# Optimization experiments

Hardware: AMD Instinct MI355X
Metric: run time of the kernel (lower is better)

Reference implementation:

```python
import jax, jax.numpy as jnp
import numpy as np

B, T, C, H = 8, 2048, 1024, 64


def build_rope_cache(seq_len, dim):
    half = dim // 2
    inv_freq = 1.0 / (10000.0 ** (jnp.arange(half, dtype=jnp.float32) / half))
    t = jnp.arange(seq_len, dtype=jnp.float32)
    freqs = t[:, None] * inv_freq[None, :]          # (T, half)
    cos = jnp.repeat(jnp.cos(freqs), 2, axis=-1)    # (T, dim) interleaved
    sin = jnp.repeat(jnp.sin(freqs), 2, axis=-1)
    return cos, sin


def apply_rope(x, cos, sin):
    # x: (B, T, H); cos/sin: (T, H)
    x1 = x[..., ::2]
    x2 = x[..., 1::2]
    rot = jnp.stack([-x2, x1], axis=-1).reshape(x.shape)
    return x * cos[None] + rot * sin[None]


def setup_inputs() -> dict:
    key = jax.random.key(0)
    kx, kq, kk, kv = jax.random.split(key, 4)
    scale = 1.0 / np.sqrt(C)
    return {
        "x": jax.random.normal(kx, (B, T, C), dtype=jnp.float32),
        "Wq": jax.random.normal(kq, (C, H), dtype=jnp.float32) * scale,
        "Wk": jax.random.normal(kk, (C, H), dtype=jnp.float32) * scale,
        "Wv": jax.random.normal(kv, (C, H), dtype=jnp.float32) * scale,
    }


def reference(x, Wq, Wk, Wv):
    Bc, Tc, _ = x.shape
    head_size = Wq.shape[1]
    cos, sin = build_rope_cache(Tc, head_size)

    q = apply_rope(x @ Wq, cos, sin)   # (B, T, H)
    k = apply_rope(x @ Wk, cos, sin)   # (B, T, H)
    v = x @ Wv                          # (B, T, H)

    # full TxT masked softmax attention (matches original non-fused path)
    wei = jnp.einsum('bth,bsh->bts', q, k) * (head_size ** -0.5)  # (B, T, T)
    causal = jnp.tril(jnp.ones((Tc, Tc), dtype=bool))
    wei = jnp.where(causal[None], wei, -jnp.inf)
    wei = jax.nn.softmax(wei, axis=-1)
    # dropout p=0 (eval mode) -> identity
    return jnp.einsum('bts,bsh->bth', wei, v)
```

## Files before the change

kernel.cpp:

```cpp
#include <hip/hip_runtime.h>
#include <cmath>

#define Tn  2048
#define Cn  1024
#define Hn  64
#define BTn 16384

typedef _Float16 f16x8 __attribute__((ext_vector_type(8)));
typedef _Float16 f16x4 __attribute__((ext_vector_type(4)));
typedef _Float16 f16x2 __attribute__((ext_vector_type(2)));
typedef float    f32x4 __attribute__((ext_vector_type(4)));

#define MFMA16(a, b, c) __builtin_amdgcn_mfma_f32_16x16x32_f16(a, b, c, 0, 0, 0)

__global__ __launch_bounds__(256) void prep_w_kernel(
    const float* __restrict__ Wq, const float* __restrict__ Wk,
    const float* __restrict__ Wv, _Float16* __restrict__ Wt)
{
    __shared__ float ts[64][65];
    const int blk = blockIdx.x;
    const int p   = blk >> 4;
    const int c0  = (blk & 15) * 64;
    const float* __restrict__ W = (p == 0) ? Wq : (p == 1) ? Wk : Wv;
    const int tid = threadIdx.x;
    #pragma unroll
    for (int it = 0; it < 16; it++) {
        int idx = tid + it * 256;
        int c = idx >> 6, n = idx & 63;
        ts[c][n] = W[(size_t)(c0 + c) * Hn + n];
    }
    __syncthreads();
    #pragma unroll
    for (int it = 0; it < 16; it++) {
        int idx = tid + it * 256;
        int n = idx >> 6, c = idx & 63;
        Wt[(size_t)(p * 64 + n) * Cn + c0 + c] = (_Float16)ts[c][n];
    }
}

#define XSP 1032

__global__ __launch_bounds__(512, 4) void proj_kernel(
    const float* __restrict__ x, const _Float16* __restrict__ Wt,
    _Float16* __restrict__ qh, _Float16* __restrict__ kh_out, _Float16* __restrict__ vT)
{
    __shared__ __align__(16) _Float16 xs[32 * XSP];
    const int row0 = blockIdx.x * 32;
    const int tid  = threadIdx.x;
    const int wave = tid >> 6, lane = tid & 63;
    const int kh   = wave >> 2;
    const int wc   = wave & 3;
    const int quad = lane >> 4, l15 = lane & 15;

    {
        float4 xv[16];
        #pragma unroll
        for (int it = 0; it < 16; it++) {
            int idx = tid + it * 512;
            int r = idx >> 8, c4 = idx & 255;
            xv[it] = *(const float4*)&x[(size_t)(row0 + r) * Cn + c4 * 4];
        }
        #pragma unroll
        for (int it = 0; it < 16; it++) {
            int idx = tid + it * 512;
            int r = idx >> 8, c4 = idx & 255;
            f16x4 hv = { (_Float16)xv[it].x, (_Float16)xv[it].y,
                         (_Float16)xv[it].z, (_Float16)xv[it].w };
            *(f16x4*)&xs[r * XSP + c4 * 4] = hv;
        }
    }
    __syncthreads();

    f32x4 acc[2][3] = {};
    const _Float16* __restrict__ wb = Wt + (size_t)(wc * 48 + l15) * Cn
                                         + kh * 512 + quad * 8;
    const _Float16* __restrict__ xp = &xs[kh * 512 + quad * 8];

    f16x8 bb[3][3], ab[3][2];
    #pragma unroll
    for (int p = 0; p < 3; p++) {
        bb[p][0] = *(const f16x8*)&wb[p * 32];
        bb[p][1] = *(const f16x8*)&wb[16 * Cn + p * 32];
        bb[p][2] = *(const f16x8*)&wb[32 * Cn + p * 32];
        ab[p][0] = *(const f16x8*)&xp[(     l15) * XSP + p * 32];
        ab[p][1] = *(const f16x8*)&xp[(16 + l15) * XSP + p * 32];
    }
    #pragma unroll
    for (int kc = 0; kc < 16; kc++) {
        const int s = kc % 3;
        acc[0][0] = MFMA16(ab[s][0], bb[s][0], acc[0][0]);
        acc[1][0] = MFMA16(ab[s][1], bb[s][0], acc[1][0]);
        acc[0][1] = MFMA16(ab[s][0], bb[s][1], acc[0][1]);
        acc[1][1] = MFMA16(ab[s][1], bb[s][1], acc[1][1]);
        acc[0][2] = MFMA16(ab[s][0], bb[s][2], acc[0][2]);
        acc[1][2] = MFMA16(ab[s][1], bb[s][2], acc[1][2]);
        if (kc + 3 < 16) {
            const int kn = (kc + 3) * 32;
            bb[s][0] = *(const f16x8*)&wb[kn];
            bb[s][1] = *(const f16x8*)&wb[16 * Cn + kn];
            bb[s][2] = *(const f16x8*)&wb[32 * Cn + kn];
            ab[s][0] = *(const f16x8*)&xp[(     l15) * XSP + kn];
            ab[s][1] = *(const f16x8*)&xp[(16 + l15) * XSP + kn];
        }
    }

    __syncthreads();
    f32x4* __restrict__ pbuf = (f32x4*)xs;
    if (kh) {
        #pragma unroll
        for (int mt = 0; mt < 2; mt++)
            #pragma unroll
            for (int nt = 0; nt < 3; nt++)
                pbuf[(mt * 3 + nt) * 256 + wc * 64 + lane] = acc[mt][nt];
    }
    __syncthreads();
    if (kh) return;
    #pragma unroll
    for (int mt = 0; mt < 2; mt++)
        #pragma unroll
        for (int nt = 0; nt < 3; nt++)
            acc[mt][nt] += pbuf[(mt * 3 + nt) * 256 + wc * 64 + lane];

    const int bidx = row0 >> 11;
    #pragma unroll
    for (int nt = 0; nt < 3; nt++) {
        const int n = wc * 48 + nt * 16 + l15;
        const int p = n >> 6;
        const int h = n & 63;
        if (p < 2) {
            _Float16* __restrict__ outb = (p == 0) ? qh : kh_out;
            const float invf = __expf(-0.2878231366242557f * (float)(h >> 1));
            #pragma unroll
            for (int mt = 0; mt < 2; mt++) {
                #pragma unroll
                for (int r = 0; r < 4; r++) {
                    int   row = row0 + mt * 16 + quad * 4 + r;
                    float val = acc[mt][nt][r];
                    float partner = __shfl_xor(val, 1, 64);
                    float ang = (float)(row & (Tn - 1)) * invf;
                    float sv, cv;
                    __sincosf(ang, &sv, &cv);
                    float res = (h & 1) ? fmaf(val, cv,  partner * sv)
                                        : fmaf(val, cv, -partner * sv);
                    if (p == 0) res *= 0.125f;
                    float resn = __shfl_xor(res, 1, 64);
                    if (!(l15 & 1)) {
                        f16x2 pk = { (_Float16)res, (_Float16)resn };
                        *(f16x2*)&outb[(size_t)row * Hn + h] = pk;
                    }
                }
            }
        } else {
            #pragma unroll
            for (int mt = 0; mt < 2; mt++) {
                int t = (row0 & (Tn - 1)) + mt * 16 + quad * 4;
                f16x4 pv = { (_Float16)acc[mt][nt][0], (_Float16)acc[mt][nt][1],
                             (_Float16)acc[mt][nt][2], (_Float16)acc[mt][nt][3] };
                *(f16x4*)&vT[((size_t)bidx * Hn + h) * Tn + t] = pv;
            }
        }
    }
}

#define PSP 72

__global__ __launch_bounds__(256, 4) void attn_kernel(
    const _Float16* __restrict__ qh, const _Float16* __restrict__ kh,
    const _Float16* __restrict__ vT, float* __restrict__ out)
{
    __shared__ _Float16 ps[4][16 * PSP];
    __shared__ float ocomb[4][16][65];
    __shared__ float mlcomb[4][2][16];

    const int blk = blockIdx.x;
    const int b   = blk & 7;
    const int j   = blk >> 3;
    const int jm  = j & 31, g = j >> 5;
    const int qt  = (g == 0) ? (127 - jm)
                  : (g == 1) ? (64 + jm)
                  : (g == 2) ? (63 - jm) : jm;
    const int t0  = qt * 16;
    const int tid = threadIdx.x;
    const int w = tid >> 6, lane = tid & 63;
    const int quad = lane >> 4, l15 = lane & 15;

    const _Float16* __restrict__ qb = qh + (size_t)b * Tn * Hn;
    const _Float16* __restrict__ kb = kh + (size_t)b * Tn * Hn;
    const _Float16* __restrict__ vb = vT + (size_t)b * Hn * Tn;

    const f16x8 aq0 = *(const f16x8*)&qb[(size_t)(t0 + l15) * Hn +      quad * 8];
    const f16x8 aq1 = *(const f16x8*)&qb[(size_t)(t0 + l15) * Hn + 32 + quad * 8];

    float m_run[4], l_run[4];
    f32x4 oacc[4] = {};
    #pragma unroll
    for (int r = 0; r < 4; r++) { m_run[r] = -1e30f; l_run[r] = 0.0f; }

    const int nst = (t0 + 16 + 63) >> 6;

    f16x8 kfA[4][2];
    if (w < nst) {
        const int s0 = w * 64;
        #pragma unroll
        for (int nt = 0; nt < 4; nt++) {
            const _Float16* kp = &kb[(size_t)(s0 + nt * 16 + l15) * Hn + quad * 8];
            kfA[nt][0] = *(const f16x8*)kp;
            kfA[nt][1] = *(const f16x8*)(kp + 32);
        }
    }

    for (int jt = w; jt < nst; jt += 4) {
        const int s0 = jt * 64;

        f16x8 vf[2][4];
        #pragma unroll
        for (int sc = 0; sc < 2; sc++)
            #pragma unroll
            for (int ht = 0; ht < 4; ht++)
                vf[sc][ht] = *(const f16x8*)&vb[(size_t)(ht * 16 + l15) * Tn
                                                + s0 + sc * 32 + quad * 8];

        f16x8 kfB[4][2];
        {
            const int sp = (jt + 4 < nst) ? (jt + 4) * 64 : s0;
            #pragma unroll
            for (int nt = 0; nt < 4; nt++) {
                const _Float16* kp = &kb[(size_t)(sp + nt * 16 + l15) * Hn + quad * 8];
                kfB[nt][0] = *(const f16x8*)kp;
                kfB[nt][1] = *(const f16x8*)(kp + 32);
            }
        }

        f32x4 sacc[4];
        #pragma unroll
        for (int nt = 0; nt < 4; nt++) {
            f32x4 z = {};
            z = MFMA16(aq0, kfA[nt][0], z);
            z = MFMA16(aq1, kfA[nt][1], z);
            sacc[nt] = z;
        }

        if (jt == nst - 1) {
            #pragma unroll
            for (int nt = 0; nt < 4; nt++)
                #pragma unroll
                for (int r = 0; r < 4; r++) {
                    int scol = s0 + nt * 16 + l15;
                    int trow = t0 + quad * 4 + r;
                    if (scol > trow) sacc[nt][r] = -1e30f;
                }
        }

        float pr[4][4];
        #pragma unroll
        for (int r = 0; r < 4; r++) {
            float mx = fmaxf(fmaxf(sacc[0][r], sacc[1][r]),
                             fmaxf(sacc[2][r], sacc[3][r]));
            #pragma unroll
            for (int off = 1; off < 16; off <<= 1)
                mx = fmaxf(mx, __shfl_xor(mx, off, 64));
            float mnew  = fmaxf(m_run[r], mx);
            float alpha = __expf(m_run[r] - mnew);
            m_run[r] = mnew;
            float rs = 0.0f;
            #pragma unroll
            for (int nt = 0; nt < 4; nt++) {
                float pv = __expf(sacc[nt][r] - mnew);
                pr[nt][r] = pv; rs += pv;
            }
            #pragma unroll
            for (int off = 1; off < 16; off <<= 1)
                rs += __shfl_xor(rs, off, 64);
            l_run[r] = fmaf(l_run[r], alpha, rs);
            #pragma unroll
            for (int ht = 0; ht < 4; ht++)
                oacc[ht][r] = oacc[ht][r] * alpha;
        }

        #pragma unroll
        for (int nt = 0; nt < 4; nt++)
            #pragma unroll
            for (int r = 0; r < 4; r++) {
                float pv = pr[nt][r];
                float pn = __shfl_xor(pv, 1, 64);
                if (!(l15 & 1)) {
                    f16x2 pk = { (_Float16)pv, (_Float16)pn };
                    *(f16x2*)&ps[w][(quad * 4 + r) * PSP + nt * 16 + l15] = pk;
                }
            }

        #pragma unroll
        for (int sc = 0; sc < 2; sc++) {
            f16x8 ap = *(const f16x8*)&ps[w][l15 * PSP + sc * 32 + quad * 8];
            #pragma unroll
            for (int ht = 0; ht < 4; ht++)
                oacc[ht] = MFMA16(ap, vf[sc][ht], oacc[ht]);
        }

        #pragma unroll
        for (int nt = 0; nt < 4; nt++) {
            kfA[nt][0] = kfB[nt][0];
            kfA[nt][1] = kfB[nt][1];
        }
    }

    #pragma unroll
    for (int r = 0; r < 4; r++) {
        #pragma unroll
        for (int ht = 0; ht < 4; ht++)
            ocomb[w][quad * 4 + r][ht * 16 + l15] = oacc[ht][r];
        if (l15 == 0) {
            mlcomb[w][0][quad * 4 + r] = m_run[r];
            mlcomb[w][1][quad * 4 + r] = l_run[r];
        }
    }
    __syncthreads();

    #pragma unroll
    for (int rp = 0; rp < 4; rp++) {
        int row = w * 4 + rp;
        float m0 = mlcomb[0][0][row], m1 = mlcomb[1][0][row];
        float m2 = mlcomb[2][0][row], m3 = mlcomb[3][0][row];
        float mm = fmaxf(fmaxf(m0, m1), fmaxf(m2, m3));
        float a0 = __expf(m0 - mm), a1 = __expf(m1 - mm);
        float a2 = __expf(m2 - mm), a3 = __expf(m3 - mm);
        float ll = mlcomb[0][1][row] * a0 + mlcomb[1][1][row] * a1
                 + mlcomb[2][1][row] * a2 + mlcomb[3][1][row] * a3;
        float ov = (ocomb[0][row][lane] * a0 + ocomb[1][row][lane] * a1
                  + ocomb[2][row][lane] * a2 + ocomb[3][row][lane] * a3) / ll;
        out[((size_t)b * Tn + t0 + row) * Hn + lane] = ov;
    }
}

extern "C" void kernel_launch(void* const* d_in, const int* in_sizes, int n_in,
                              void* d_out, int out_size, void* d_ws, size_t ws_size,
                              hipStream_t stream) {
    const float* x  = (const float*)d_in[0];
    const float* Wq = (const float*)d_in[1];
    const float* Wk = (const float*)d_in[2];
    const float* Wv = (const float*)d_in[3];

    const size_t qkvN = (size_t)BTn * Hn;
    _Float16* qh = (_Float16*)d_ws;
    _Float16* kh = qh + qkvN;
    _Float16* vT = kh + qkvN;
    _Float16* Wt = vT + qkvN;

    prep_w_kernel<<<48, 256, 0, stream>>>(Wq, Wk, Wv, Wt);
    proj_kernel<<<BTn / 32, 512, 0, stream>>>(x, Wt, qh, kh, vT);
    attn_kernel<<<1024, 256, 0, stream>>>(qh, kh, vT, (float*)d_out);
}
```

Baseline: 176.9 us.

## Fuse weight prep, projection and attention into one persistent kernel with grid barriers

```diff
diff --git a/kernel.cpp b/kernel.cpp
--- a/kernel.cpp
+++ b/kernel.cpp
@@ -13,322 +13,318 @@
 
 #define MFMA16(a, b, c) __builtin_amdgcn_mfma_f32_16x16x32_f16(a, b, c, 0, 0, 0)
 
-__global__ __launch_bounds__(256) void prep_w_kernel(
-    const float* __restrict__ Wq, const float* __restrict__ Wk,
-    const float* __restrict__ Wv, _Float16* __restrict__ Wt)
+#define XSP 1032
+#define PSP 72
+#define SUBSZ 26368
+
+__device__ __forceinline__ void gbar(unsigned* cnt)
 {
-    __shared__ float ts[64][65];
-    const int blk = blockIdx.x;
-    const int p   = blk >> 4;
-    const int c0  = (blk & 15) * 64;
-    const float* __restrict__ W = (p == 0) ? Wq : (p == 1) ? Wk : Wv;
-    const int tid = threadIdx.x;
-    #pragma unroll
-    for (int it = 0; it < 16; it++) {
-        int idx = tid + it * 256;
-        int c = idx >> 6, n = idx & 63;
-        ts[c][n] = W[(size_t)(c0 + c) * Hn + n];
+    __syncthreads();
+    if (threadIdx.x == 0) {
+        __threadfence();
+        unsigned prev   = atomicAdd(cnt, 1u);
+        unsigned target = (prev / gridDim.x + 1u) * gridDim.x;
+        for (int i = 0; i < (1 << 24); i++) {
+            if (atomicAdd(cnt, 0u) >= target) break;
+            __builtin_amdgcn_s_sleep(1);
+        }
+        __threadfence();
     }
     __syncthreads();
-    #pragma unroll
-    for (int it = 0; it < 16; it++) {
-        int idx = tid + it * 256;
-        int n = idx >> 6, c = idx & 63;
-        Wt[(size_t)(p * 64 + n) * Cn + c0 + c] = (_Float16)ts[c][n];
+}
+
+__global__ __launch_bounds__(512, 4) void fused_kernel(
+    const float* __restrict__ x,  const float* __restrict__ Wq,
+    const float* __restrict__ Wk, const float* __restrict__ Wv,
+    _Float16* __restrict__ qh, _Float16* __restrict__ kh_g,
+    _Float16* __restrict__ vT, _Float16* __restrict__ Wt,
+    float* __restrict__ out, unsigned* __restrict__ cnt)
+{
+    __shared__ __align__(16) char smem[66048];
+    const int tid  = threadIdx.x;
+    const int blk  = blockIdx.x;
+    const int lane = tid & 63;
+    const int quad = lane >> 4, l15 = lane & 15;
+
+    if (blk < 48) {
+        float (*ts)[65] = (float (*)[65])smem;
+        const int p  = blk >> 4;
+        const int c0 = (blk & 15) * 64;
+        const float* __restrict__ W = (p == 0) ? Wq : (p == 1) ? Wk : Wv;
+        #pragma unroll
+        for (int it = 0; it < 8; it++) {
+            int idx = tid + it * 512;
+            int c = idx >> 6, n = idx & 63;
+            ts[c][n] = W[(size_t)(c0 + c) * Hn + n];
+        }
+        __syncthreads();
+        #pragma unroll
+        for (int it = 0; it < 8; it++) {
+            int idx = tid + it * 512;
+            int n = idx >> 6, c = idx & 63;
+            Wt[(size_t)(p * 64 + n) * Cn + c0 + c] = (_Float16)ts[c][n];
+        }
     }
-}
-
-#define XSP 1032
-
-__global__ __launch_bounds__(512, 4) void proj_kernel(
-    const float* __restrict__ x, const _Float16* __restrict__ Wt,
-    _Float16* __restrict__ qh, _Float16* __restrict__ kh_out, _Float16* __restrict__ vT)
-{
-    __shared__ __align__(16) _Float16 xs[32 * XSP];
-    const int row0 = blockIdx.x * 32;
-    const int tid  = threadIdx.x;
-    const int wave = tid >> 6, lane = tid & 63;
-    const int kh   = wave >> 2;
-    const int wc   = wave & 3;
-    const int quad = lane >> 4, l15 = lane & 15;
+    gbar(cnt);
 
     {
-        float4 xv[16];
-        #pragma unroll
-        for (int it = 0; it < 16; it++) {
-            int idx = tid + it * 512;
-            int r = idx >> 8, c4 = idx & 255;
-            xv[it] = *(const float4*)&x[(size_t)(row0 + r) * Cn + c4 * 4];
-        }
-        #pragma unroll
-        for (int it = 0; it < 16; it++) {
-            int idx = tid + it * 512;
-            int r = idx >> 8, c4 = idx & 255;
-            f16x4 hv = { (_Float16)xv[it].x, (_Float16)xv[it].y,
-                         (_Float16)xv[it].z, (_Float16)xv[it].w };
-            *(f16x4*)&xs[r * XSP + c4 * 4] = hv;
-        }
-    }
-    __syncthreads();
-
-    f32x4 acc[2][3] = {};
-    const _Float16* __restrict__ wb = Wt + (size_t)(wc * 48 + l15) * Cn
-                                         + kh * 512 + quad * 8;
-    const _Float16* __restrict__ xp = &xs[kh * 512 + quad * 8];
-
-    f16x8 bb[3][3], ab[3][2];
-    #pragma unroll
-    for (int p = 0; p < 3; p++) {
-        bb[p][0] = *(const f16x8*)&wb[p * 32];
-        bb[p][1] = *(const f16x8*)&wb[16 * Cn + p * 32];
-        bb[p][2] = *(const f16x8*)&wb[32 * Cn + p * 32];
-        ab[p][0] = *(const f16x8*)&xp[(     l15) * XSP + p * 32];
-        ab[p][1] = *(const f16x8*)&xp[(16 + l15) * XSP + p * 32];
-    }
-    #pragma unroll
-    for (int kc = 0; kc < 16; kc++) {
-        const int s = kc % 3;
-        acc[0][0] = MFMA16(ab[s][0], bb[s][0], acc[0][0]);
-        acc[1][0] = MFMA16(ab[s][1], bb[s][0], acc[1][0]);
-        acc[0][1] = MFMA16(ab[s][0], bb[s][1], acc[0][1]);
-        acc[1][1] = MFMA16(ab[s][1], bb[s][1], acc[1][1]);
-        acc[0][2] = MFMA16(ab[s][0], bb[s][2], acc[0][2]);
-        acc[1][2] = MFMA16(ab[s][1], bb[s][2], acc[1][2]);
-        if (kc + 3 < 16) {
-            const int kn = (kc + 3) * 32;
-            bb[s][0] = *(const f16x8*)&wb[kn];
-            bb[s][1] = *(const f16x8*)&wb[16 * Cn + kn];
-            bb[s][2] = *(const f16x8*)&wb[32 * Cn + kn];
-            ab[s][0] = *(const f16x8*)&xp[(     l15) * XSP + kn];
-            ab[s][1] = *(const f16x8*)&xp[(16 + l15) * XSP + kn];
-        }
-    }
-
-    __syncthreads();
-    f32x4* __restrict__ pbuf = (f32x4*)xs;
-    if (kh) {
-        #pragma unroll
-        for (int mt = 0; mt < 2; mt++)
-            #pragma unroll
-            for (int nt = 0; nt < 3; nt++)
-                pbuf[(mt * 3 + nt) * 256 + wc * 64 + lane] = acc[mt][nt];
-    }
-    __syncthreads();
-    if (kh) return;
-    #pragma unroll
-    for (int mt = 0; mt < 2; mt++)
-        #pragma unroll
-        for (int nt = 0; nt < 3; nt++)
-            acc[mt][nt] += pbuf[(mt * 3 + nt) * 256 + wc * 64 + lane];
-
-    const int bidx = row0 >> 11;
-    #pragma unroll
-    for (int nt = 0; nt < 3; nt++) {
-        const int n = wc * 48 + nt * 16 + l15;
-        const int p = n >> 6;
-        const int h = n & 63;
-        if (p < 2) {
-            _Float16* __restrict__ outb = (p == 0) ? qh : kh_out;
-            const float invf = __expf(-0.2878231366242557f * (float)(h >> 1));
-            #pragma unroll
-            for (int mt = 0; mt < 2; mt++) {
-                #pragma unroll
-                for (int r = 0; r < 4; r++) {
-                    int   row = row0 + mt * 16 + quad * 4 + r;
-                    float val = acc[mt][nt][r];
-                    float partner = __shfl_xor(val, 1, 64);
-                    float ang = (float)(row & (Tn - 1)) * invf;
-                    float sv, cv;
-                    __sincosf(ang, &sv, &cv);
-                    float res = (h & 1) ? fmaf(val, cv,  partner * sv)
-                                        : fmaf(val, cv, -partner * sv);
-                    if (p == 0) res *= 0.125f;
-                    float resn = __shfl_xor(res, 1, 64);
-                    if (!(l15 & 1)) {
-                        f16x2 pk = { (_Float16)res, (_Float16)resn };
-                        *(f16x2*)&outb[(size_t)row * Hn + h] = pk;
+        _Float16* xs = (_Float16*)smem;
+        const int row0  = blk * 32;
+        const int wave  = tid >> 6;
+        const int khalf = wave >> 2;
+        const int wc    = wave & 3;
+
+        {
+            float4 xv[16];
+            #pragma unroll
+            for (int it = 0; it < 16; it++) {
+                int idx = tid + it * 512;
+                int r = idx >> 8, c4 = idx & 255;
+                xv[it] = *(const float4*)&x[(size_t)(row0 + r) * Cn + c4 * 4];
+            }
+            #pragma unroll
+            for (int it = 0; it < 16; it++) {
+                int idx = tid + it * 512;
+                int r = idx >> 8, c4 = idx & 255;
+                f16x4 hv = { (_Float16)xv[it].x, (_Float16)xv[it].y,
+                             (_Float16)xv[it].z, (_Float16)xv[it].w };
+                *(f16x4*)&xs[r * XSP + c4 * 4] = hv;
+            }
+        }
+        __syncthreads();
+
+        f32x4 acc[2][3] = {};
+        const _Float16* __restrict__ wb = Wt + (size_t)(wc * 48 + l15) * Cn
+                                             + khalf * 512 + quad * 8;
+        const _Float16* __restrict__ xp = &xs[khalf * 512 + quad * 8];
+
+        f16x8 bb[3][3], ab[3][2];
+        #pragma unroll
+        for (int p = 0; p < 3; p++) {
+            bb[p][0] = *(const f16x8*)&wb[p * 32];
+            bb[p][1] = *(const f16x8*)&wb[16 * Cn + p * 32];
+            bb[p][2] = *(const f16x8*)&wb[32 * Cn + p * 32];
+            ab[p][0] = *(const f16x8*)&xp[(     l15) * XSP + p * 32];
+            ab[p][1] = *(const f16x8*)&xp[(16 + l15) * XSP + p * 32];
+        }
+        #pragma unroll
+        for (int kc = 0; kc < 16; kc++) {
+            const int s = kc % 3;
+            acc[0][0] = MFMA16(ab[s][0], bb[s][0], acc[0][0]);
+            acc[1][0] = MFMA16(ab[s][1], bb[s][0], acc[1][0]);
+            acc[0][1] = MFMA16(ab[s][0], bb[s][1], acc[0][1]);
+            acc[1][1] = MFMA16(ab[s][1], bb[s][1], acc[1][1]);
+            acc[0][2] = MFMA16(ab[s][0], bb[s][2], acc[0][2]);
+            acc[1][2] = MFMA16(ab[s][1], bb[s][2], acc[1][2]);
+            if (kc + 3 < 16) {
+                const int kn = (kc + 3) * 32;
+                bb[s][0] = *(const f16x8*)&wb[kn];
+                bb[s][1] = *(const f16x8*)&wb[16 * Cn + kn];
+                bb[s][2] = *(const f16x8*)&wb[32 * Cn + kn];
+                ab[s][0] = *(const f16x8*)&xp[(     l15) * XSP + kn];
+                ab[s][1] = *(const f16x8*)&xp[(16 + l15) * XSP + kn];
+            }
+        }
+
+        __syncthreads();
+        f32x4* __restrict__ pbuf = (f32x4*)smem;
+        if (khalf) {
+            #pragma unroll
+            for (int mt = 0; mt < 2; mt++)
+                #pragma unroll
+                for (int nt = 0; nt < 3; nt++)
+                    pbuf[(mt * 3 + nt) * 256 + wc * 64 + lane] = acc[mt][nt];
+        }
+        __syncthreads();
+        if (!khalf) {
+            #pragma unroll
+            for (int mt = 0; mt < 2; mt++)
+                #pragma unroll
+                for (int nt = 0; nt < 3; nt++)
+                    acc[mt][nt] += pbuf[(mt * 3 + nt) * 256 + wc * 64 + lane];
+
+            const int bidx = row0 >> 11;
+            #pragma unroll
+            for (int nt = 0; nt < 3; nt++) {
+                const int n = wc * 48 + nt * 16 + l15;
+                const int p = n >> 6;
+                const int h = n & 63;
+                if (p < 2) {
+                    _Float16* __restrict__ outb = (p == 0) ? qh : kh_g;
+                    const float invf = __expf(-0.2878231366242557f * (float)(h >> 1));
+                    #pragma unroll
+                    for (int mt = 0; mt < 2; mt++) {
+                        #pragma unroll
+                        for (int r = 0; r < 4; r++) {
+                            int   row = row0 + mt * 16 + quad * 4 + r;
+                            float val = acc[mt][nt][r];
+                            float partner = __shfl_xor(val, 1, 64);
+                            float ang = (float)(row & (Tn - 1)) * invf;
+                            float sv, cv;
+                            __sincosf(ang, &sv, &cv);
+                            float res = (h & 1) ? fmaf(val, cv,  partner * sv)
+                                                : fmaf(val, cv, -partner * sv);
+                            if (p == 0) res *= 0.125f;
+                            float resn = __shfl_xor(res, 1, 64);
+                            if (!(l15 & 1)) {
+                                f16x2 pk = { (_Float16)res, (_Float16)resn };
+                                *(f16x2*)&outb[(size_t)row * Hn + h] = pk;
+                            }
+                        }
+                    }
+                } else {
+                    #pragma unroll
+                    for (int mt = 0; mt < 2; mt++) {
+                        int t = (row0 & (Tn - 1)) + mt * 16 + quad * 4;
+                        f16x4 pv = { (_Float16)acc[mt][nt][0], (_Float16)acc[mt][nt][1],
+                                     (_Float16)acc[mt][nt][2], (_Float16)acc[mt][nt][3] };
+                        *(f16x4*)&vT[((size_t)bidx * Hn + h) * Tn + t] = pv;
                     }
                 }
             }
-        } else {
-            #pragma unroll
-            for (int mt = 0; mt < 2; mt++) {
-                int t = (row0 & (Tn - 1)) + mt * 16 + quad * 4;
-                f16x4 pv = { (_Float16)acc[mt][nt][0], (_Float16)acc[mt][nt][1],
-                             (_Float16)acc[mt][nt][2], (_Float16)acc[mt][nt][3] };
-                *(f16x4*)&vT[((size_t)bidx * Hn + h) * Tn + t] = pv;
-            }
         }
     }
-}
-
-#define PSP 72
-
-__global__ __launch_bounds__(256, 4) void attn_kernel(
-    const _Float16* __restrict__ qh, const _Float16* __restrict__ kh,
-    const _Float16* __restrict__ vT, float* __restrict__ out)
-{
-    __shared__ _Float16 ps[4][16 * PSP];
-    __shared__ float ocomb[4][16][65];
-    __shared__ float mlcomb[4][2][16];
-
-    const int blk = blockIdx.x;
-    const int b   = blk & 7;
-    const int j   = blk >> 3;
-    const int jm  = j & 31, g = j >> 5;
-    const int qt  = (g == 0) ? (127 - jm)
-                  : (g == 1) ? (64 + jm)
-                  : (g == 2) ? (63 - jm) : jm;
-    const int t0  = qt * 16;
-    const int tid = threadIdx.x;
-    const int w = tid >> 6, lane = tid & 63;
-    const int quad = lane >> 4, l15 = lane & 15;
-
-    const _Float16* __restrict__ qb = qh + (size_t)b * Tn * Hn;
-    const _Float16* __restrict__ kb = kh + (size_t)b * Tn * Hn;
-    const _Float16* __restrict__ vb = vT + (size_t)b * Hn * Tn;
-
-    const f16x8 aq0 = *(const f16x8*)&qb[(size_t)(t0 + l15) * Hn +      quad * 8];
-    const f16x8 aq1 = *(const f16x8*)&qb[(size_t)(t0 + l15) * Hn + 32 + quad * 8];
-
-    float m_run[4], l_run[4];
-    f32x4 oacc[4] = {};
-    #pragma unroll
-    for (int r = 0; r < 4; r++) { m_run[r] = -1e30f; l_run[r] = 0.0f; }
-
-    const int nst = (t0 + 16 + 63) >> 6;
-
-    f16x8 kfA[4][2];
-    if (w < nst) {
-        const int s0 = w * 64;
-        #pragma unroll
-        for (int nt = 0; nt < 4; nt++) {
-            const _Float16* kp = &kb[(size_t)(s0 + nt * 16 + l15) * Hn + quad * 8];
-            kfA[nt][0] = *(const f16x8*)kp;
-            kfA[nt][1] = *(const f16x8*)(kp + 32);
-        }
-    }
-
-    for (int jt = w; jt < nst; jt += 4) {
-        const int s0 = jt * 64;
-
-        f16x8 vf[2][4];
-        #pragma unroll
-        for (int sc = 0; sc < 2; sc++)
+    gbar(cnt);
+
+    {
+        const int sub  = tid >> 8;
+        const int stid = tid & 255;
+        const int w    = stid >> 6;
+        const int m    = blk >> 3;
+        const int b    = blk & 7;
+        const int qt   = sub ? (127 - m) : m;
+        const int t0   = qt * 16;
+
+        _Float16* ps  = (_Float16*)(smem + sub * SUBSZ);
+        float*    ocm = (float*)  (smem + sub * SUBSZ + 9216);
+        float*    mlc = (float*)  (smem + sub * SUBSZ + 9216 + 16640);
+
+        const _Float16* __restrict__ qb = qh   + (size_t)b * Tn * Hn;
+        const _Float16* __restrict__ kb = kh_g + (size_t)b * Tn * Hn;
+        const _Float16* __restrict__ vb = vT   + (size_t)b * Hn * Tn;
+
+        const f16x8 aq0 = *(const f16x8*)&qb[(size_t)(t0 + l15) * Hn +      quad * 8];
+        const f16x8 aq1 = *(const f16x8*)&qb[(size_t)(t0 + l15) * Hn + 32 + quad * 8];
+
+        float m_run[4], l_run[4];
+        f32x4 oacc[4] = {};
+        #pragma unroll
+        for (int r = 0; r < 4; r++) { m_run[r] = -1e30f; l_run[r] = 0.0f; }
+
+        const int nst = (t0 + 16 + 63) >> 6;
+        for (int jt = w; jt < nst; jt += 4) {
+            const int s0 = jt * 64;
+
+            f16x8 kf[4][2];
+            #pragma unroll
+            for (int nt = 0; nt < 4; nt++) {
+                const _Float16* kp = &kb[(size_t)(s0 + nt * 16 + l15) * Hn + quad * 8];
+                kf[nt][0] = *(const f16x8*)kp;
+                kf[nt][1] = *(const f16x8*)(kp + 32);
+            }
+            f32x4 sacc[4];
+            #pragma unroll
+            for (int nt = 0; nt < 4; nt++) {
+                f32x4 z = {};
+                z = MFMA16(aq0, kf[nt][0], z);
+                z = MFMA16(aq1, kf[nt][1], z);
+                sacc[nt] = z;
+            }
+
+            f16x8 vf[2][4];
+            #pragma unroll
+            for (int sc = 0; sc < 2; sc++)
+                #pragma unroll
+                for (int ht = 0; ht < 4; ht++)
+                    vf[sc][ht] = *(const f16x8*)&vb[(size_t)(ht * 16 + l15) * Tn
+                                                    + s0 + sc * 32 + quad * 8];
+
+            if (jt == nst - 1) {
+                #pragma unroll
+                for (int nt = 0; nt < 4; nt++)
+                    #pragma unroll
+                    for (int r = 0; r < 4; r++) {
+                        int scol = s0 + nt * 16 + l15;
+                        int trow = t0 + quad * 4 + r;
+                        if (scol > trow) sacc[nt][r] = -1e30f;
+                    }
+            }
+
+            float pr[4][4];
+            #pragma unroll
+            for (int r = 0; r < 4; r++) {
+                float mx = fmaxf(fmaxf(sacc[0][r], sacc[1][r]),
+                                 fmaxf(sacc[2][r], sacc[3][r]));
+                #pragma unroll
+                for (int off = 1; off < 16; off <<= 1)
+                    mx = fmaxf(mx, __shfl_xor(mx, off, 64));
+                float mnew  = fmaxf(m_run[r], mx);
+                float alpha = __expf(m_run[r] - mnew);
+                m_run[r] = mnew;
+                float rs = 0.0f;
+                #pragma unroll
+                for (int nt = 0; nt < 4; nt++) {
+                    float pv = __expf(sacc[nt][r] - mnew);
+                    pr[nt][r] = pv; rs += pv;
+                }
+                #pragma unroll
+                for (int off = 1; off < 16; off <<= 1)
+                    rs += __shfl_xor(rs, off, 64);
+                l_run[r] = fmaf(l_run[r], alpha, rs);
+                #pragma unroll
+                for (int ht = 0; ht < 4; ht++)
+                    oacc[ht][r] = oacc[ht][r] * alpha;
+            }
+
+            #pragma unroll
+            for (int nt = 0; nt < 4; nt++)
+                #pragma unroll
+                for (int r = 0; r < 4; r++) {
+                    float pv = pr[nt][r];
+                    float pn = __shfl_xor(pv, 1, 64);
+                    if (!(l15 & 1)) {
+                        f16x2 pk = { (_Float16)pv, (_Float16)pn };
+                        *(f16x2*)&ps[w * 16 * PSP + (quad * 4 + r) * PSP + nt * 16 + l15] = pk;
+                    }
+                }
+
+            #pragma unroll
+            for (int sc = 0; sc < 2; sc++) {
+                f16x8 ap = *(const f16x8*)&ps[w * 16 * PSP + l15 * PSP + sc * 32 + quad * 8];
+                #pragma unroll
+                for (int ht = 0; ht < 4; ht++)
+                    oacc[ht] = MFMA16(ap, vf[sc][ht], oacc[ht]);
+            }
+        }
+
+        #pragma unroll
+        for (int r = 0; r < 4; r++) {
             #pragma unroll
             for (int ht = 0; ht < 4; ht++)
-                vf[sc][ht] = *(const f16x8*)&vb[(size_t)(ht * 16 + l15) * Tn
-                                                + s0 + sc * 32 + quad * 8];
-
-        f16x8 kfB[4][2];
-        {
-            const int sp = (jt + 4 < nst) ? (jt + 4) * 64 : s0;
-            #pragma unroll
-            for (int nt = 0; nt < 4; nt++) {
-                const _Float16* kp = &kb[(size_t)(sp + nt * 16 + l15) * Hn + quad * 8];
-                kfB[nt][0] = *(const f16x8*)kp;
-                kfB[nt][1] = *(const f16x8*)(kp + 32);
-            }
-        }
-
-        f32x4 sacc[4];
-        #pragma unroll
-        for (int nt = 0; nt < 4; nt++) {
-            f32x4 z = {};
-            z = MFMA16(aq0, kfA[nt][0], z);
-            z = MFMA16(aq1, kfA[nt][1], z);
-            sacc[nt] = z;
-        }
-
-        if (jt == nst - 1) {
-            #pragma unroll
-            for (int nt = 0; nt < 4; nt++)
-                #pragma unroll
-                for (int r = 0; r < 4; r++) {
-                    int scol = s0 + nt * 16 + l15;
-                    int trow = t0 + quad * 4 + r;
-                    if (scol > trow) sacc[nt][r] = -1e30f;
-                }
-        }
-
-        float pr[4][4];
-        #pragma unroll
-        for (int r = 0; r < 4; r++) {
-            float mx = fmaxf(fmaxf(sacc[0][r], sacc[1][r]),
-                             fmaxf(sacc[2][r], sacc[3][r]));
-            #pragma unroll
-            for (int off = 1; off < 16; off <<= 1)
-                mx = fmaxf(mx, __shfl_xor(mx, off, 64));
-            float mnew  = fmaxf(m_run[r], mx);
-            float alpha = __expf(m_run[r] - mnew);
-            m_run[r] = mnew;
-            float rs = 0.0f;
-            #pragma unroll
-            for (int nt = 0; nt < 4; nt++) {
-                float pv = __expf(sacc[nt][r] - mnew);
-                pr[nt][r] = pv; rs += pv;
-            }
-            #pragma unroll
-            for (int off = 1; off < 16; off <<= 1)
-                rs += __shfl_xor(rs, off, 64);
-            l_run[r] = fmaf(l_run[r], alpha, rs);
-            #pragma unroll
-            for (int ht = 0; ht < 4; ht++)
-                oacc[ht][r] = oacc[ht][r] * alpha;
-        }
-
-        #pragma unroll
-        for (int nt = 0; nt < 4; nt++)
-            #pragma unroll
-            for (int r = 0; r < 4; r++) {
-                float pv = pr[nt][r];
-                float pn = __shfl_xor(pv, 1, 64);
-                if (!(l15 & 1)) {
-                    f16x2 pk = { (_Float16)pv, (_Float16)pn };
-                    *(f16x2*)&ps[w][(quad * 4 + r) * PSP + nt * 16 + l15] = pk;
-                }
-            }
-
-        #pragma unroll
-        for (int sc = 0; sc < 2; sc++) {
-            f16x8 ap = *(const f16x8*)&ps[w][l15 * PSP + sc * 32 + quad * 8];
-            #pragma unroll
-            for (int ht = 0; ht < 4; ht++)
-                oacc[ht] = MFMA16(ap, vf[sc][ht], oacc[ht]);
-        }
-
-        #pragma unroll
-        for (int nt = 0; nt < 4; nt++) {
-            kfA[nt][0] = kfB[nt][0];
-            kfA[nt][1] = kfB[nt][1];
-        }
-    }
-
-    #pragma unroll
-    for (int r = 0; r < 4; r++) {
-        #pragma unroll
-        for (int ht = 0; ht < 4; ht++)
-            ocomb[w][quad * 4 + r][ht * 16 + l15] = oacc[ht][r];
-        if (l15 == 0) {
-            mlcomb[w][0][quad * 4 + r] = m_run[r];
-            mlcomb[w][1][quad * 4 + r] = l_run[r];
-        }
-    }
-    __syncthreads();
-
-    #pragma unroll
-    for (int rp = 0; rp < 4; rp++) {
-        int row = w * 4 + rp;
-        float m0 = mlcomb[0][0][row], m1 = mlcomb[1][0][row];
-        float m2 = mlcomb[2][0][row], m3 = mlcomb[3][0][row];
-        float mm = fmaxf(fmaxf(m0, m1), fmaxf(m2, m3));
-        float a0 = __expf(m0 - mm), a1 = __expf(m1 - mm);
-        float a2 = __expf(m2 - mm), a3 = __expf(m3 - mm);
-        float ll = mlcomb[0][1][row] * a0 + mlcomb[1][1][row] * a1
-                 + mlcomb[2][1][row] * a2 + mlcomb[3][1][row] * a3;
-        float ov = (ocomb[0][row][lane] * a0 + ocomb[1][row][lane] * a1
-                  + ocomb[2][row][lane] * a2 + ocomb[3][row][lane] * a3) / ll;
-        out[((size_t)b * Tn + t0 + row) * Hn + lane] = ov;
+                ocm[(w * 16 + quad * 4 + r) * 65 + ht * 16 + l15] = oacc[ht][r];
+            if (l15 == 0) {
+                mlc[(w * 2 + 0) * 16 + quad * 4 + r] = m_run[r];
+                mlc[(w * 2 + 1) * 16 + quad * 4 + r] = l_run[r];
+            }
+        }
+        __syncthreads();
+
+        #pragma unroll
+        for (int rp = 0; rp < 4; rp++) {
+            int row = w * 4 + rp;
+            float m0 = mlc[(0) * 16 + row], m1 = mlc[(2) * 16 + row];
+            float m2 = mlc[(4) * 16 + row], m3 = mlc[(6) * 16 + row];
+            float mm = fmaxf(fmaxf(m0, m1), fmaxf(m2, m3));
+            float a0 = __expf(m0 - mm), a1 = __expf(m1 - mm);
+            float a2 = __expf(m2 - mm), a3 = __expf(m3 - mm);
+            float ll = mlc[(1) * 16 + row] * a0 + mlc[(3) * 16 + row] * a1
+                     + mlc[(5) * 16 + row] * a2 + mlc[(7) * 16 + row] * a3;
+            float ov = (ocm[(0 * 16 + row) * 65 + lane] * a0
+                      + ocm[(1 * 16 + row) * 65 + lane] * a1
+                      + ocm[(2 * 16 + row) * 65 + lane] * a2
+                      + ocm[(3 * 16 + row) * 65 + lane] * a3) / ll;
+            out[((size_t)b * Tn + t0 + row) * Hn + lane] = ov;
+        }
     }
 }
 
@@ -345,8 +341,10 @@
     _Float16* kh = qh + qkvN;
     _Float16* vT = kh + qkvN;
     _Float16* Wt = vT + qkvN;
-
-    prep_w_kernel<<<48, 256, 0, stream>>>(Wq, Wk, Wv, Wt);
-    proj_kernel<<<BTn / 32, 512, 0, stream>>>(x, Wt, qh, kh, vT);
-    attn_kernel<<<1024, 256, 0, stream>>>(qh, kh, vT, (float*)d_out);
+    unsigned* cnt = (unsigned*)(Wt + (size_t)192 * Cn);
+    float*    op  = (float*)d_out;
+
+    hipMemsetAsync(cnt, 0, 128, stream);
+    hipLaunchKernelGGL(fused_kernel, dim3(512), dim3(512), 0, stream,
+                       x, Wq, Wk, Wv, qh, kh, vT, Wt, op, cnt);
 }
```

Result: slower. 254.6 us (+44.0%).
